# Optimization experiments

Measured on AMD Instinct MI355X. Metric: run time of the kernel, lower is better.

The kernel has to match this reference:

```python
import jax, jax.numpy as jnp
import numpy as np

B, S, HID = 1, 2048, 2048
H, KV, D = 16, 8, 128          # heads, kv heads, head_dim
EPS = 1e-6
THETA_T, THETA_HW = 1000000.0, 10000.0
SCALE = D ** -0.5
NEG = -1e9


def _rms(x, w):
    xf = x.astype(jnp.float32)
    var = jnp.mean(xf * xf, axis=-1, keepdims=True)
    return (w * (xf * jax.lax.rsqrt(var + EPS))).astype(x.dtype)


def _rope_cs(pos, theta, half_dim):
    # Module builds RoPE with head_dim = 2*half_dim then takes every-other freq:
    # exponents arange(0, 2*half_dim, 4) / (2*half_dim)  -> half_dim//2 freqs
    dim2 = 2 * half_dim
    inv_freq = 1.0 / theta ** (jnp.arange(0, dim2, 4, dtype=jnp.float32) / dim2)
    freqs = pos.astype(jnp.float32)[:, None] * inv_freq[None, :]   # [S, half_dim//2]
    emb = jnp.concatenate([freqs, freqs], axis=-1)                 # [S, half_dim]
    return jnp.cos(emb), jnp.sin(emb)


def _rot_half(x):
    d = x.shape[-1] // 2
    return jnp.concatenate([-x[..., d:], x[..., :d]], axis=-1)


def _apply_rope(q, k, cos, sin):
    cos = cos[None, None]  # [1,1,S,dim]
    sin = sin[None, None]
    return q * cos + _rot_half(q) * sin, k * cos + _rot_half(k) * sin


def setup_inputs() -> dict:
    key = jax.random.key(0)
    ks = jax.random.split(key, 10)
    hidden_states = jax.random.normal(ks[0], (B, S, HID), jnp.float32)
    indexes = jax.random.randint(ks[1], (3, S), 0, S)
    causal = jnp.tril(jnp.ones((S, S), bool))
    attention_mask = jnp.where(causal, 0.0, NEG).astype(jnp.float32)[None, None]
    qkv_w = jax.random.normal(ks[2], ((H + 2 * KV) * D, HID), jnp.float32) * 0.02
    qkv_b = jax.random.normal(ks[3], ((H + 2 * KV) * D,), jnp.float32) * 0.02
    o_w = jax.random.normal(ks[4], (HID, H * D), jnp.float32) * 0.02
    o_b = jax.random.normal(ks[5], (HID,), jnp.float32) * 0.02
    q_norm_w = jnp.ones((D // 2,), jnp.float32)
    k_norm_w = jnp.ones((D // 2,), jnp.float32)
    q_norm_hw_w = jnp.ones((D // 2,), jnp.float32)
    k_norm_hw_w = jnp.ones((D // 2,), jnp.float32)
    return dict(hidden_states=hidden_states, indexes=indexes, attention_mask=attention_mask,
                qkv_w=qkv_w, qkv_b=qkv_b, o_w=o_w, o_b=o_b,
                q_norm_w=q_norm_w, k_norm_w=k_norm_w,
                q_norm_hw_w=q_norm_hw_w, k_norm_hw_w=k_norm_hw_w)


def reference(hidden_states, indexes, attention_mask, qkv_w, qkv_b, o_w, o_b,
              q_norm_w, k_norm_w, q_norm_hw_w, k_norm_hw_w):
    b, s, _ = hidden_states.shape
    qkv = hidden_states @ qkv_w.T + qkv_b
    q, k, v = jnp.split(qkv, [H * D, H * D + KV * D], axis=-1)
    q = q.reshape(b, s, H, D)
    k = k.reshape(b, s, KV, D)
    v = v.reshape(b, s, KV, D)

    # split head_dim into time half and hw half
    q_t, q_hw = jnp.split(q, 2, axis=-1)
    k_t, k_hw = jnp.split(k, 2, axis=-1)
    q_t = jnp.swapaxes(_rms(q_t, q_norm_w), 1, 2)       # [B,H,S,D/2]
    k_t = jnp.swapaxes(_rms(k_t, k_norm_w), 1, 2)
    q_hw = jnp.swapaxes(_rms(q_hw, q_norm_hw_w), 1, 2)
    k_hw = jnp.swapaxes(_rms(k_hw, k_norm_hw_w), 1, 2)
    q_h, q_ww = jnp.split(q_hw, 2, axis=-1)             # [B,H,S,D/4]
    k_h, k_ww = jnp.split(k_hw, 2, axis=-1)

    cos_t, sin_t = _rope_cs(indexes[0], THETA_T, D // 2)
    q_t, k_t = _apply_rope(q_t, k_t, cos_t, sin_t)
    cos_h, sin_h = _rope_cs(indexes[1], THETA_HW, D // 4)
    q_h, k_h = _apply_rope(q_h, k_h, cos_h, sin_h)
    cos_w, sin_w = _rope_cs(indexes[2], THETA_HW, D // 4)
    q_ww, k_ww = _apply_rope(q_ww, k_ww, cos_w, sin_w)

    query = jnp.concatenate([q_t, q_h, q_ww], axis=-1)  # [B,H,S,D]
    keyst = jnp.concatenate([k_t, k_h, k_ww], axis=-1)  # [B,KV,S,D]
    value = jnp.swapaxes(v, 1, 2)                       # [B,KV,S,D]

    n_rep = H // KV
    keyst = jnp.repeat(keyst, n_rep, axis=1)
    value = jnp.repeat(value, n_rep, axis=1)

    scores = jnp.einsum('bhsd,bhtd->bhst', query, keyst) * SCALE + attention_mask
    probs = jax.nn.softmax(scores.astype(jnp.float32), axis=-1).astype(query.dtype)
    attn = jnp.einsum('bhst,bhtd->bhsd', probs, value)
    attn = jnp.swapaxes(attn, 1, 2).reshape(b, s, H * D)
    return attn @ o_w.T + o_b
```

## Files before the change

kernel.cpp:

```cpp
#include <hip/hip_runtime.h>

typedef __bf16 bf16;
typedef __bf16 bf16x4 __attribute__((ext_vector_type(4)));
typedef __bf16 bf16x8 __attribute__((ext_vector_type(8)));
typedef float f32x4 __attribute__((ext_vector_type(4)));

#define S_LEN 2048
#define HIDDEN 2048
#define NH 16
#define NKV 8
#define HD 128
#define QKV_N 4096

#define PSLOT 66560

__device__ __forceinline__ void async_load16(const void* g, void* l) {
  __builtin_amdgcn_global_load_lds((const __attribute__((address_space(1))) unsigned int*)g,
                                   (__attribute__((address_space(3))) unsigned int*)l,
                                   16, 0, 0);
}

template <int C>
__device__ __forceinline__ float dpp_f(float x) {
  return __builtin_bit_cast(float, __builtin_amdgcn_mov_dpp(
      __builtin_bit_cast(int, x), C, 0xF, 0xF, true));
}
__device__ __forceinline__ float rowmax16(float x) {
  x = fmaxf(x, dpp_f<0x128>(x));
  x = fmaxf(x, dpp_f<0x124>(x));
  x = fmaxf(x, dpp_f<0x122>(x));
  x = fmaxf(x, dpp_f<0x121>(x));
  return x;
}
__device__ __forceinline__ float rowsum16(float x) {
  x += dpp_f<0x128>(x);
  x += dpp_f<0x124>(x);
  x += dpp_f<0x122>(x);
  x += dpp_f<0x121>(x);
  return x;
}

__global__ __launch_bounds__(256)
void cvt_f32_bf16(const float* __restrict__ src, bf16* __restrict__ dst, int n) {
  int i = (blockIdx.x * 256 + threadIdx.x) * 4;
  if (i < n) {
    float4 v = *(const float4*)(src + i);
    bf16x4 o = {(bf16)v.x, (bf16)v.y, (bf16)v.z, (bf16)v.w};
    *(bf16x4*)(dst + i) = o;
  }
}

__global__ __launch_bounds__(256)
void cvt_pair(const float* __restrict__ s1, bf16* __restrict__ d1, int n1,
              const float* __restrict__ s2, bf16* __restrict__ d2, int n2) {
  int i = (blockIdx.x * 256 + threadIdx.x) * 4;
  const float* s;
  bf16* d;
  int j;
  if (i < n1) { s = s1; d = d1; j = i; }
  else        { s = s2; d = d2; j = i - n1; if (j >= n2) return; }
  float4 v = *(const float4*)(s + j);
  bf16x4 o = {(bf16)v.x, (bf16)v.y, (bf16)v.z, (bf16)v.w};
  *(bf16x4*)(d + j) = o;
}

template <int WRITE_BF16>
__global__ __launch_bounds__(256)
void gemm_bt(const bf16* __restrict__ A, const bf16* __restrict__ B,
             const float* __restrict__ bias, void* __restrict__ Cout,
             int M, int N, int K) {
  __shared__ bf16 As[2][128 * 64];
  __shared__ bf16 Bs[2][128 * 64];
  const int tid = threadIdx.x;
  const int w = tid >> 6, lane = tid & 63;
  const int quad = lane >> 4, l15 = lane & 15;
  const int wm = w >> 1, wn = w & 1;
  const int m0 = blockIdx.y * 128, n0 = blockIdx.x * 128;

  f32x4 acc[4][4];
#pragma unroll
  for (int i = 0; i < 4; i++)
#pragma unroll
    for (int j = 0; j < 4; j++) acc[i][j] = (f32x4){0.f, 0.f, 0.f, 0.f};

  const int crow = lane >> 2;
  const int ccol = (lane & 3) * 8;

#pragma unroll
  for (int q = 0; q < 4; q++) {
    int c = w * 4 + q, rb = c >> 1, kh = c & 1;
    async_load16(A + (size_t)(m0 + rb * 16 + crow) * K + kh * 32 + ccol,
                 (char*)As[0] + c * 1024);
    async_load16(B + (size_t)(n0 + rb * 16 + crow) * K + kh * 32 + ccol,
                 (char*)Bs[0] + c * 1024);
  }

  int cur = 0;
  for (int k0 = 0; k0 < K; k0 += 64) {
    __asm__ __volatile__("s_waitcnt vmcnt(0)" ::: "memory");
    __syncthreads();
    if (k0 + 64 < K) {
#pragma unroll
      for (int q = 0; q < 4; q++) {
        int c = w * 4 + q, rb = c >> 1, kh = c & 1;
        async_load16(A + (size_t)(m0 + rb * 16 + crow) * K + k0 + 64 + kh * 32 + ccol,
                     (char*)As[cur ^ 1] + c * 1024);
        async_load16(B + (size_t)(n0 + rb * 16 + crow) * K + k0 + 64 + kh * 32 + ccol,
                     (char*)Bs[cur ^ 1] + c * 1024);
      }
    }
    bf16x8 af[4][2], bfr[4][2];
#pragma unroll
    for (int i = 0; i < 4; i++)
#pragma unroll
      for (int kk = 0; kk < 2; kk++)
        af[i][kk] = *(const bf16x8*)((const char*)As[cur] +
                                     ((wm * 4 + i) * 2 + kk) * 1024 + l15 * 64 + quad * 16);
#pragma unroll
    for (int j = 0; j < 4; j++)
#pragma unroll
      for (int kk = 0; kk < 2; kk++)
        bfr[j][kk] = *(const bf16x8*)((const char*)Bs[cur] +
                                      ((wn * 4 + j) * 2 + kk) * 1024 + l15 * 64 + quad * 16);
#pragma unroll
    for (int kk = 0; kk < 2; kk++)
#pragma unroll
      for (int i = 0; i < 4; i++)
#pragma unroll
        for (int j = 0; j < 4; j++)
          acc[i][j] = __builtin_amdgcn_mfma_f32_16x16x32_bf16(af[i][kk], bfr[j][kk],
                                                              acc[i][j], 0, 0, 0);
    cur ^= 1;
  }

#pragma unroll
  for (int i = 0; i < 4; i++) {
#pragma unroll
    for (int j = 0; j < 4; j++) {
      int col = n0 + wn * 64 + j * 16 + l15;
      float bv = bias[col];
#pragma unroll
      for (int r = 0; r < 4; r++) {
        int row = m0 + wm * 64 + i * 16 + quad * 4 + r;
        float v = acc[i][j][r] + bv;
        if (WRITE_BF16)
          ((bf16*)Cout)[(size_t)row * N + col] = (bf16)v;
        else
          ((float*)Cout)[(size_t)row * N + col] = v;
      }
    }
  }
}

__global__ __launch_bounds__(128)
void normrope(const bf16* __restrict__ qkv, const int* __restrict__ idx,
              const float* __restrict__ qnw, const float* __restrict__ knw,
              const float* __restrict__ qnhw, const float* __restrict__ knhw,
              bf16* __restrict__ Qb, bf16* __restrict__ Kb) {
  const int y = blockIdx.y;
  const int d = threadIdx.x;

  const bool isq = (y < 16);
  const int off = isq ? (y * HD + d) : (2048 + (y - 16) * HD + d);
  const float* wt = (d < 64) ? (isq ? qnw : knw) : (isq ? qnhw : knhw);
  const float wv = wt[d & 63];

  float invf;
  int xorm, posrow;
  bool firsthalf;
  if (d < 64) {
    int i = d & 31;
    invf = exp2f(-(float)i * 0.6228615177913804f);
    xorm = 32;
    firsthalf = (d < 32);
    posrow = 0;
  } else {
    int j = d - 64;
    int region = j >> 5;
    int i = j & 15;
    invf = exp2f(-(float)i * 0.8304820237218406f);
    xorm = 16;
    firsthalf = ((j & 31) < 16);
    posrow = 1 + region;
  }

  bf16* outp = isq ? (Qb + ((size_t)y * S_LEN) * HD + d)
                   : (Kb + ((size_t)(y - 16) * S_LEN) * HD + d);
  const float oscale = isq ? 0.12751745f : 1.0f;

#pragma unroll
  for (int si = 0; si < 8; si++) {
    const int s = blockIdx.x * 8 + si;
    float x = (float)qkv[(size_t)s * QKV_N + off];

    float ss = x * x;
#pragma unroll
    for (int o = 32; o; o >>= 1) ss += __shfl_xor(ss, o);
    float inv = rsqrtf(ss * (1.f / 64.f) + 1e-6f);
    float yn = x * inv * wv;

    float pos = (float)idx[posrow * S_LEN + s];
    float ang = pos * invf;
    float si_, co;
    sincosf(ang, &si_, &co);
    float partner = __shfl_xor(yn, xorm);
    float outv = firsthalf ? (yn * co - partner * si_) : (yn * co + partner * si_);
    outp[(size_t)s * HD] = (bf16)(outv * oscale);
  }
}

__global__ __launch_bounds__(256)
void vtrans(const bf16* __restrict__ qkv, bf16* __restrict__ VT) {
  __shared__ bf16 T[64][72];
  const int tid = threadIdx.x;
  const int s0 = blockIdx.x * 64, d0 = blockIdx.y * 64, kv = blockIdx.z;
#pragma unroll
  for (int it = 0; it < 2; it++) {
    int r = (tid >> 3) + it * 32;
    int c = (tid & 7) * 8;
    bf16x8 v = *(const bf16x8*)(qkv + (size_t)(s0 + r) * QKV_N + 3072 + kv * HD + d0 + c);
    *(bf16x8*)(&T[r][c]) = v;
  }
  __syncthreads();
#pragma unroll
  for (int it = 0; it < 2; it++) {
    int r = (tid >> 3) + it * 32;
    int c = (tid & 7) * 8;
    bf16x8 o;
#pragma unroll
    for (int j = 0; j < 8; j++) o[j] = T[c + j][r];
    *(bf16x8*)(VT + ((size_t)kv * HD + d0 + r) * S_LEN + s0 + c) = o;
  }
}

__global__ __launch_bounds__(256)
void attn_fused(const bf16* __restrict__ Qb, const bf16* __restrict__ Kb,
                const bf16* __restrict__ VT, bf16* __restrict__ attnO,
                char* __restrict__ Opart) {
  __shared__ bf16 Kbuf[2][8192];
  __shared__ bf16 Vbuf[8192];
  __shared__ __align__(16) bf16 Ps[4][2][16][72];
  const int tid = threadIdx.x;
  const int w = tid >> 6, lane = tid & 63;
  const int quad = lane >> 4, l15 = lane & 15;
  const int b = blockIdx.x;
  const int h = b & 15;
  const int cid = b >> 4;
  int G, c, nc;
  if (cid < 7)       { G = cid;          c = 0;     nc = 1; }
  else if (cid < 21) { int t = cid - 7;  G = 7 + (t >> 1);  c = t & 1; nc = 2; }
  else               { int t = cid - 21; G = 14 + t / 3;    c = t % 3; nc = 3; }
  const int nT = 2 * G + 2;
  const int tBeg = c * 14;
  const int tEnd = (tBeg + 14 < nT) ? (tBeg + 14) : nT;
  const int tCap0 = 2 * G + 1;
  const int kv = h >> 1;
  const int qr0h[2] = {G * 128 + w * 16, G * 128 + 64 + w * 16};

  const bf16* Qg = Qb + (size_t)h * S_LEN * HD;
  const bf16* Kg = Kb + (size_t)kv * S_LEN * HD;
  const bf16* Vg = VT + (size_t)kv * HD * S_LEN;

  const bf16* ksrc = Kg + (size_t)(w * 16 + l15) * HD + quad * 8;
  const bf16* vsrc = Vg + (size_t)(2 * w * 16 + l15) * S_LEN + quad * 8;

  bf16x8 aq[2][4];
#pragma unroll
  for (int bb = 0; bb < 2; bb++)
#pragma unroll
    for (int kc = 0; kc < 4; kc++)
      aq[bb][kc] = *(const bf16x8*)(Qg + (size_t)(qr0h[bb] + l15) * HD + kc * 32 + quad * 8);

  float m2[2][4], li[2][4];
  f32x4 Oacc[2][8];
#pragma unroll
  for (int bb = 0; bb < 2; bb++) {
#pragma unroll
    for (int r = 0; r < 4; r++) { m2[bb][r] = -1e30f; li[bb][r] = 0.f; }
#pragma unroll
    for (int dt = 0; dt < 8; dt++) Oacc[bb][dt] = (f32x4){0.f, 0.f, 0.f, 0.f};
  }

#pragma unroll
  for (int kc = 0; kc < 4; kc++)
    async_load16(ksrc + (size_t)(tBeg << 6) * HD + kc * 32,
                 (char*)Kbuf[tBeg & 1] + (w * 4 + kc) * 1024);

  for (int tt = tBeg; tt < tEnd; ++tt) {
    const int t0 = tt << 6;
    const int cur = tt & 1;
    const bool more = (tt + 1 < tEnd);
    const bool do0 = (tt < tCap0);
    __asm__ __volatile__("s_waitcnt vmcnt(0)" ::: "memory");
    __syncthreads();

#pragma unroll
    for (int e = 0; e < 2; e++)
#pragma unroll
      for (int half = 0; half < 2; half++)
        async_load16(vsrc + (size_t)e * 16 * S_LEN + t0 + half * 32,
                     (char*)Vbuf + (half * 8 + 2 * w + e) * 1024);
    if (more) {
#pragma unroll
      for (int kc = 0; kc < 4; kc++)
        async_load16(ksrc + (size_t)(t0 + 64) * HD + kc * 32,
                     (char*)Kbuf[cur ^ 1] + (w * 4 + kc) * 1024);
    }

#pragma unroll
    for (int bb = 0; bb < 2; bb++) {
      if (bb == 0 && !do0) continue;
      const int qr0 = qr0h[bb];
      f32x4 sacc[4];
#pragma unroll
      for (int nt = 0; nt < 4; nt++) {
        sacc[nt] = (f32x4){0.f, 0.f, 0.f, 0.f};
#pragma unroll
        for (int kc = 0; kc < 4; kc++) {
          bf16x8 bk = *(const bf16x8*)((const char*)Kbuf[cur] + (nt * 4 + kc) * 1024 + lane * 16);
          sacc[nt] = __builtin_amdgcn_mfma_f32_16x16x32_bf16(aq[bb][kc], bk, sacc[nt], 0, 0, 0);
        }
      }
      const bool full = (t0 + 64 <= qr0);
      float mxv[4];
      bool need = false;
#pragma unroll
      for (int r = 0; r < 4; r++) {
        if (!full) {
          const int mrow = qr0 + quad * 4 + r;
          const int cb = t0 + l15;
          if (cb > mrow) sacc[0][r] = -1e30f;
          if (cb + 16 > mrow) sacc[1][r] = -1e30f;
          if (cb + 32 > mrow) sacc[2][r] = -1e30f;
          if (cb + 48 > mrow) sacc[3][r] = -1e30f;
        }
        mxv[r] = rowmax16(fmaxf(fmaxf(sacc[0][r], sacc[1][r]), fmaxf(sacc[2][r], sacc[3][r])));
        need = need || (mxv[r] > m2[bb][r] + 8.f);
      }
      if (__any(need ? 1 : 0)) {
#pragma unroll
        for (int r = 0; r < 4; r++) {
          float mnew = fmaxf(m2[bb][r], mxv[r]);
          float a = exp2f(m2[bb][r] - mnew);
          li[bb][r] *= a;
#pragma unroll
          for (int dt = 0; dt < 8; dt++) Oacc[bb][dt][r] *= a;
          m2[bb][r] = mnew;
        }
      }
#pragma unroll
      for (int r = 0; r < 4; r++) {
        float p0 = exp2f(sacc[0][r] - m2[bb][r]);
        float p1 = exp2f(sacc[1][r] - m2[bb][r]);
        float p2 = exp2f(sacc[2][r] - m2[bb][r]);
        float p3 = exp2f(sacc[3][r] - m2[bb][r]);
        li[bb][r] += rowsum16((p0 + p1) + (p2 + p3));
        Ps[w][bb][quad * 4 + r][l15] = (bf16)p0;
        Ps[w][bb][quad * 4 + r][16 + l15] = (bf16)p1;
        Ps[w][bb][quad * 4 + r][32 + l15] = (bf16)p2;
        Ps[w][bb][quad * 4 + r][48 + l15] = (bf16)p3;
      }
    }
    __asm__ __volatile__("s_waitcnt lgkmcnt(0)" ::: "memory");
    if (more)
      __asm__ __volatile__("s_waitcnt vmcnt(4)" ::: "memory");
    else
      __asm__ __volatile__("s_waitcnt vmcnt(0)" ::: "memory");

#pragma unroll
    for (int bb = 0; bb < 2; bb++) {
      if (bb == 0 && !do0) continue;
#pragma unroll
      for (int half = 0; half < 2; half++) {
        bf16x8 ap = *(const bf16x8*)(&Ps[w][bb][l15][half * 32 + quad * 8]);
#pragma unroll
        for (int dt = 0; dt < 8; dt++) {
          bf16x8 bv = *(const bf16x8*)((const char*)Vbuf + (half * 8 + dt) * 1024 + lane * 16);
          Oacc[bb][dt] = __builtin_amdgcn_mfma_f32_16x16x32_bf16(ap, bv, Oacc[bb][dt], 0, 0, 0);
        }
      }
    }
  }

  if (nc > 1) {
    char* slot = Opart + (size_t)((cid - 7) * 16 + h) * PSLOT;
    float* Op = (float*)slot;
    float* mlp = (float*)(slot + 65536);
#pragma unroll
    for (int bb = 0; bb < 2; bb++) {
#pragma unroll
      for (int r = 0; r < 4; r++) {
        const int row = bb * 64 + w * 16 + quad * 4 + r;
#pragma unroll
        for (int dt = 0; dt < 8; dt++)
          Op[row * 128 + dt * 16 + l15] = Oacc[bb][dt][r];
        if (l15 == 0) {
          mlp[row * 2 + 0] = m2[bb][r];
          mlp[row * 2 + 1] = li[bb][r];
        }
      }
    }
  } else {
#pragma unroll
    for (int bb = 0; bb < 2; bb++) {
#pragma unroll
      for (int r = 0; r < 4; r++) {
        float invl = 1.f / li[bb][r];
        int srow = qr0h[bb] + quad * 4 + r;
#pragma unroll
        for (int dt = 0; dt < 8; dt++)
          attnO[(size_t)srow * HIDDEN + h * HD + dt * 16 + l15] = (bf16)(Oacc[bb][dt][r] * invl);
      }
    }
  }
}

__global__ __launch_bounds__(256)
void attn_merge(const char* __restrict__ Opart, bf16* __restrict__ attnO) {
  const int h = blockIdx.x & 15;
  const int idx = blockIdx.x >> 4;
  int G, nc, cid0;
  if (idx < 7) { G = 7 + idx;        nc = 2; cid0 = 7 + idx * 2; }
  else         { G = 14 + (idx - 7); nc = 3; cid0 = 21 + (idx - 7) * 3; }
  const char* s0 = Opart + (size_t)((cid0 - 7) * 16 + h) * PSLOT;
  const char* s1 = s0 + (size_t)16 * PSLOT;
  const char* s2 = s0 + (size_t)32 * PSLOT;
  const float* O0 = (const float*)s0;
  const float* O1 = (const float*)s1;
  const float* O2 = (const float*)s2;
  const float* ML0 = (const float*)(s0 + 65536);
  const float* ML1 = (const float*)(s1 + 65536);
  const float* ML2 = (const float*)(s2 + 65536);
  const int t = threadIdx.x;
#pragma unroll
  for (int it = 0; it < 16; ++it) {
    int e = it * 256 + t;
    int row = e >> 5, d = (e & 31) * 4;
    float m0 = ML0[row * 2], l0 = ML0[row * 2 + 1];
    float m1 = ML1[row * 2], l1 = ML1[row * 2 + 1];
    float m2v = -1e30f, l2v = 0.f;
    if (nc == 3) { m2v = ML2[row * 2]; l2v = ML2[row * 2 + 1]; }
    float m = fmaxf(fmaxf(m0, m1), m2v);
    float a0 = exp2f(m0 - m), a1 = exp2f(m1 - m), a2 = exp2f(m2v - m);
    float inv = 1.f / (a0 * l0 + a1 * l1 + a2 * l2v);
    f32x4 x0 = *(const f32x4*)(O0 + row * 128 + d);
    f32x4 x1 = *(const f32x4*)(O1 + row * 128 + d);
    f32x4 x2 = (f32x4){0.f, 0.f, 0.f, 0.f};
    if (nc == 3) x2 = *(const f32x4*)(O2 + row * 128 + d);
    int srow = G * 128 + row;
    bf16x4 o;
#pragma unroll
    for (int j = 0; j < 4; j++)
      o[j] = (bf16)((a0 * x0[j] + a1 * x1[j] + a2 * x2[j]) * inv);
    *(bf16x4*)(attnO + (size_t)srow * HIDDEN + h * HD + d) = o;
  }
}

extern "C" void kernel_launch(void* const* d_in, const int* in_sizes, int n_in,
                              void* d_out, int out_size, void* d_ws, size_t ws_size,
                              hipStream_t stream) {
  const float* hidden = (const float*)d_in[0];
  const int* idx = (const int*)d_in[1];
  const float* qkv_w = (const float*)d_in[3];
  const float* qkv_b = (const float*)d_in[4];
  const float* o_w = (const float*)d_in[5];
  const float* o_b = (const float*)d_in[6];
  const float* qnw = (const float*)d_in[7];
  const float* knw = (const float*)d_in[8];
  const float* qnhw = (const float*)d_in[9];
  const float* knhw = (const float*)d_in[10];

  char* ws = (char*)d_ws;
  bf16* hB    = (bf16*)(ws);
  bf16* qwB   = (bf16*)(ws + (8u << 20));
  bf16* qkvB  = (bf16*)(ws + (24u << 20));
  bf16* Qb    = (bf16*)(ws + (40u << 20));
  bf16* Kb    = (bf16*)(ws + (48u << 20));
  bf16* VT    = (bf16*)(ws + (52u << 20));
  bf16* owB   = hB;
  char* Opart = ws + (8u << 20);
  bf16* attn  = (bf16*)(ws + (32u << 20));

  cvt_pair<<<12288, 256, 0, stream>>>(hidden, hB, HIDDEN * S_LEN,
                                      qkv_w, qwB, QKV_N * HIDDEN);

  gemm_bt<1><<<dim3(QKV_N / 128, S_LEN / 128), 256, 0, stream>>>(
      hB, qwB, qkv_b, qkvB, S_LEN, QKV_N, HIDDEN);

  cvt_f32_bf16<<<HIDDEN * HIDDEN / 1024, 256, 0, stream>>>(o_w, owB, HIDDEN * HIDDEN);

  normrope<<<dim3(S_LEN / 8, 24), 128, 0, stream>>>(qkvB, idx, qnw, knw, qnhw, knhw, Qb, Kb);
  vtrans<<<dim3(S_LEN / 64, HD / 64, NKV), 256, 0, stream>>>(qkvB, VT);

  attn_fused<<<432, 256, 0, stream>>>(Qb, Kb, VT, attn, Opart);
  attn_merge<<<144, 256, 0, stream>>>(Opart, attn);

  gemm_bt<0><<<dim3(HIDDEN / 128, S_LEN / 128), 256, 0, stream>>>(
      attn, owB, o_b, (float*)d_out, S_LEN, HIDDEN, HIDDEN);
}
```

Measured before the change: 300.5 us.

## Fuse RMSNorm, RoPE and V transpose into the QKV GEMM epilogue

Replaces the generic QKV GEMM plus separate normrope and vtrans kernels with a specialized GEMM whose epilogue applies bias, per-head RMSNorm (via a 16-lane row reduction), RoPE and Q scaling, and writes V directly in transposed layout. This removes the intermediate qkv buffer round-trip through global memory and two kernel launches. The epilogue gets heavier (sincos, shuffles, scattered 2-byte stores for Q/K), which may lengthen GEMM tail time.

```diff
diff --git a/kernel.cpp b/kernel.cpp
--- a/kernel.cpp
+++ b/kernel.cpp
@@ -152,84 +152,154 @@
   }
 }
 
-__global__ __launch_bounds__(128)
-void normrope(const bf16* __restrict__ qkv, const int* __restrict__ idx,
+__global__ __launch_bounds__(256)
+void gemm_qkv(const bf16* __restrict__ A, const bf16* __restrict__ B,
+              const float* __restrict__ bias, const int* __restrict__ idx,
               const float* __restrict__ qnw, const float* __restrict__ knw,
               const float* __restrict__ qnhw, const float* __restrict__ knhw,
-              bf16* __restrict__ Qb, bf16* __restrict__ Kb) {
-  const int y = blockIdx.y;
-  const int d = threadIdx.x;
-
-  const bool isq = (y < 16);
-  const int off = isq ? (y * HD + d) : (2048 + (y - 16) * HD + d);
-  const float* wt = (d < 64) ? (isq ? qnw : knw) : (isq ? qnhw : knhw);
-  const float wv = wt[d & 63];
-
-  float invf;
-  int xorm, posrow;
-  bool firsthalf;
-  if (d < 64) {
-    int i = d & 31;
-    invf = exp2f(-(float)i * 0.6228615177913804f);
-    xorm = 32;
-    firsthalf = (d < 32);
-    posrow = 0;
+              bf16* __restrict__ Qb, bf16* __restrict__ Kb, bf16* __restrict__ VT) {
+  const int K = HIDDEN;
+  __shared__ bf16 As[2][128 * 64];
+  __shared__ bf16 Bs[2][128 * 64];
+  const int tid = threadIdx.x;
+  const int w = tid >> 6, lane = tid & 63;
+  const int quad = lane >> 4, l15 = lane & 15;
+  const int wm = w >> 1, wn = w & 1;
+  const int m0 = blockIdx.y * 128, n0 = blockIdx.x * 128;
+
+  f32x4 acc[4][4];
+#pragma unroll
+  for (int i = 0; i < 4; i++)
+#pragma unroll
+    for (int j = 0; j < 4; j++) acc[i][j] = (f32x4){0.f, 0.f, 0.f, 0.f};
+
+  const int crow = lane >> 2;
+  const int ccol = (lane & 3) * 8;
+
+#pragma unroll
+  for (int q = 0; q < 4; q++) {
+    int c = w * 4 + q, rb = c >> 1, kh = c & 1;
+    async_load16(A + (size_t)(m0 + rb * 16 + crow) * K + kh * 32 + ccol,
+                 (char*)As[0] + c * 1024);
+    async_load16(B + (size_t)(n0 + rb * 16 + crow) * K + kh * 32 + ccol,
+                 (char*)Bs[0] + c * 1024);
+  }
+
+  int cur = 0;
+  for (int k0 = 0; k0 < K; k0 += 64) {
+    __asm__ __volatile__("s_waitcnt vmcnt(0)" ::: "memory");
+    __syncthreads();
+    if (k0 + 64 < K) {
+#pragma unroll
+      for (int q = 0; q < 4; q++) {
+        int c = w * 4 + q, rb = c >> 1, kh = c & 1;
+        async_load16(A + (size_t)(m0 + rb * 16 + crow) * K + k0 + 64 + kh * 32 + ccol,
+                     (char*)As[cur ^ 1] + c * 1024);
+        async_load16(B + (size_t)(n0 + rb * 16 + crow) * K + k0 + 64 + kh * 32 + ccol,
+                     (char*)Bs[cur ^ 1] + c * 1024);
+      }
+    }
+    bf16x8 af[4][2], bfr[4][2];
+#pragma unroll
+    for (int i = 0; i < 4; i++)
+#pragma unroll
+      for (int kk = 0; kk < 2; kk++)
+        af[i][kk] = *(const bf16x8*)((const char*)As[cur] +
+                                     ((wm * 4 + i) * 2 + kk) * 1024 + l15 * 64 + quad * 16);
+#pragma unroll
+    for (int j = 0; j < 4; j++)
+#pragma unroll
+      for (int kk = 0; kk < 2; kk++)
+        bfr[j][kk] = *(const bf16x8*)((const char*)Bs[cur] +
+                                      ((wn * 4 + j) * 2 + kk) * 1024 + l15 * 64 + quad * 16);
+#pragma unroll
+    for (int kk = 0; kk < 2; kk++)
+#pragma unroll
+      for (int i = 0; i < 4; i++)
+#pragma unroll
+        for (int j = 0; j < 4; j++)
+          acc[i][j] = __builtin_amdgcn_mfma_f32_16x16x32_bf16(af[i][kk], bfr[j][kk],
+                                                              acc[i][j], 0, 0, 0);
+    cur ^= 1;
+  }
+
+  const int nb = blockIdx.x;
+
+  if (nb >= 24) {
+    const int kv = nb - 24;
+#pragma unroll
+    for (int i = 0; i < 4; i++) {
+#pragma unroll
+      for (int j = 0; j < 4; j++) {
+        const int d = wn * 64 + j * 16 + l15;
+        const float bv = bias[n0 + d];
+        bf16x4 o;
+#pragma unroll
+        for (int r = 0; r < 4; r++) o[r] = (bf16)(acc[i][j][r] + bv);
+        *(bf16x4*)(VT + ((size_t)(kv * HD + d)) * S_LEN +
+                   (m0 + wm * 64 + i * 16 + quad * 4)) = o;
+      }
+    }
+    return;
+  }
+
+  const bool isq = (nb < 16);
+  const int head = isq ? nb : nb - 16;
+  const float* wt = (wn == 0) ? (isq ? qnw : knw) : (isq ? qnhw : knhw);
+  float wvj[4], bvj[4];
+#pragma unroll
+  for (int j = 0; j < 4; j++) {
+    wvj[j] = wt[j * 16 + l15];
+    bvj[j] = bias[n0 + wn * 64 + j * 16 + l15];
+  }
+  float invfA, invfB;
+  if (wn == 0) {
+    invfA = exp2f(-(float)l15 * 0.6228615177913804f);
+    invfB = exp2f(-(float)(16 + l15) * 0.6228615177913804f);
   } else {
-    int j = d - 64;
-    int region = j >> 5;
-    int i = j & 15;
-    invf = exp2f(-(float)i * 0.8304820237218406f);
-    xorm = 16;
-    firsthalf = ((j & 31) < 16);
-    posrow = 1 + region;
-  }
-
-  bf16* outp = isq ? (Qb + ((size_t)y * S_LEN) * HD + d)
-                   : (Kb + ((size_t)(y - 16) * S_LEN) * HD + d);
+    invfA = exp2f(-(float)l15 * 0.8304820237218406f);
+    invfB = invfA;
+  }
   const float oscale = isq ? 0.12751745f : 1.0f;
-
-#pragma unroll
-  for (int si = 0; si < 8; si++) {
-    const int s = blockIdx.x * 8 + si;
-    float x = (float)qkv[(size_t)s * QKV_N + off];
-
-    float ss = x * x;
-#pragma unroll
-    for (int o = 32; o; o >>= 1) ss += __shfl_xor(ss, o);
-    float inv = rsqrtf(ss * (1.f / 64.f) + 1e-6f);
-    float yn = x * inv * wv;
-
-    float pos = (float)idx[posrow * S_LEN + s];
-    float ang = pos * invf;
-    float si_, co;
-    sincosf(ang, &si_, &co);
-    float partner = __shfl_xor(yn, xorm);
-    float outv = firsthalf ? (yn * co - partner * si_) : (yn * co + partner * si_);
-    outp[(size_t)s * HD] = (bf16)(outv * oscale);
-  }
-}
-
-__global__ __launch_bounds__(256)
-void vtrans(const bf16* __restrict__ qkv, bf16* __restrict__ VT) {
-  __shared__ bf16 T[64][72];
-  const int tid = threadIdx.x;
-  const int s0 = blockIdx.x * 64, d0 = blockIdx.y * 64, kv = blockIdx.z;
-#pragma unroll
-  for (int it = 0; it < 2; it++) {
-    int r = (tid >> 3) + it * 32;
-    int c = (tid & 7) * 8;
-    bf16x8 v = *(const bf16x8*)(qkv + (size_t)(s0 + r) * QKV_N + 3072 + kv * HD + d0 + c);
-    *(bf16x8*)(&T[r][c]) = v;
-  }
-  __syncthreads();
-#pragma unroll
-  for (int it = 0; it < 2; it++) {
-    int r = (tid >> 3) + it * 32;
-    int c = (tid & 7) * 8;
-    bf16x8 o;
-#pragma unroll
-    for (int j = 0; j < 8; j++) o[j] = T[c + j][r];
-    *(bf16x8*)(VT + ((size_t)kv * HD + d0 + r) * S_LEN + s0 + c) = o;
+  bf16* outbase = (isq ? Qb : Kb) + (size_t)head * S_LEN * HD;
+
+#pragma unroll
+  for (int i = 0; i < 4; i++) {
+#pragma unroll
+    for (int r = 0; r < 4; r++) {
+      const int srow = m0 + wm * 64 + i * 16 + quad * 4 + r;
+      float v0 = acc[i][0][r] + bvj[0], v1 = acc[i][1][r] + bvj[1];
+      float v2 = acc[i][2][r] + bvj[2], v3 = acc[i][3][r] + bvj[3];
+      float ss = rowsum16(v0 * v0 + v1 * v1 + v2 * v2 + v3 * v3);
+      float inv = rsqrtf(ss * (1.f / 64.f) + 1e-6f);
+      float y0 = v0 * inv * wvj[0], y1 = v1 * inv * wvj[1];
+      float y2 = v2 * inv * wvj[2], y3 = v3 * inv * wvj[3];
+      float o0, o1, o2, o3;
+      if (wn == 0) {
+        float pos = (float)idx[srow];
+        float sA, cA, sB, cB;
+        sincosf(pos * invfA, &sA, &cA);
+        sincosf(pos * invfB, &sB, &cB);
+        o0 = y0 * cA - y2 * sA;
+        o1 = y1 * cB - y3 * sB;
+        o2 = y2 * cA + y0 * sA;
+        o3 = y3 * cB + y1 * sB;
+      } else {
+        float p1 = (float)idx[S_LEN + srow], p2 = (float)idx[2 * S_LEN + srow];
+        float s1, c1, s2, c2;
+        sincosf(p1 * invfA, &s1, &c1);
+        sincosf(p2 * invfA, &s2, &c2);
+        o0 = y0 * c1 - y1 * s1;
+        o1 = y1 * c1 + y0 * s1;
+        o2 = y2 * c2 - y3 * s2;
+        o3 = y3 * c2 + y2 * s2;
+      }
+      bf16* op = outbase + (size_t)srow * HD + wn * 64 + l15;
+      op[0]  = (bf16)(o0 * oscale);
+      op[16] = (bf16)(o1 * oscale);
+      op[32] = (bf16)(o2 * oscale);
+      op[48] = (bf16)(o3 * oscale);
+    }
   }
 }
 
@@ -473,7 +543,6 @@
   char* ws = (char*)d_ws;
   bf16* hB    = (bf16*)(ws);
   bf16* qwB   = (bf16*)(ws + (8u << 20));
-  bf16* qkvB  = (bf16*)(ws + (24u << 20));
   bf16* Qb    = (bf16*)(ws + (40u << 20));
   bf16* Kb    = (bf16*)(ws + (48u << 20));
   bf16* VT    = (bf16*)(ws + (52u << 20));
@@ -484,13 +553,10 @@
   cvt_pair<<<12288, 256, 0, stream>>>(hidden, hB, HIDDEN * S_LEN,
                                       qkv_w, qwB, QKV_N * HIDDEN);
 
-  gemm_bt<1><<<dim3(QKV_N / 128, S_LEN / 128), 256, 0, stream>>>(
-      hB, qwB, qkv_b, qkvB, S_LEN, QKV_N, HIDDEN);
+  gemm_qkv<<<dim3(QKV_N / 128, S_LEN / 128), 256, 0, stream>>>(
+      hB, qwB, qkv_b, idx, qnw, knw, qnhw, knhw, Qb, Kb, VT);
 
   cvt_f32_bf16<<<HIDDEN * HIDDEN / 1024, 256, 0, stream>>>(o_w, owB, HIDDEN * HIDDEN);
-
-  normrope<<<dim3(S_LEN / 8, 24), 128, 0, stream>>>(qkvB, idx, qnw, knw, qnhw, knhw, Qb, Kb);
-  vtrans<<<dim3(S_LEN / 64, HD / 64, NKV), 256, 0, stream>>>(qkvB, VT);
 
   attn_fused<<<432, 256, 0, stream>>>(Qb, Kb, VT, attn, Opart);
   attn_merge<<<144, 256, 0, stream>>>(Opart, attn);
```

Measured after the change: 420.4 us. 1.4x slower.
